# Kernel tuning notes

Hardware: AMD Instinct MI355X
Metric: run time of the kernel (lower is better)

Reference implementation:

```python
import jax, jax.numpy as jnp
import numpy as np

N_NODES = 50000
N_EDGES = 800000
D_FEAT = 128
HIDDEN = 128
BERT_DIM = 768
BATCH = 4096
MAX_ENT = 20
COMB = BERT_DIM + HIDDEN  # 896


def setup_inputs() -> dict:
    key = jax.random.key(0)
    ks = jax.random.split(key, 12)
    article_bert_embeddings = jax.random.normal(ks[0], (BATCH, BERT_DIM), dtype=jnp.float32)
    x = jax.random.normal(ks[1], (N_NODES, D_FEAT), dtype=jnp.float32)
    edge_index = jax.random.randint(ks[2], (2, N_EDGES), 0, N_NODES, dtype=jnp.int64)
    entity_map = jax.random.randint(ks[3], (BATCH, MAX_ENT), 0, N_NODES, dtype=jnp.int64)
    pad = jax.random.uniform(ks[4], (BATCH, MAX_ENT)) < 0.3
    entity_map = jnp.where(pad, jnp.int64(-1), entity_map)
    s = 1.0 / np.sqrt(D_FEAT)
    W1 = jax.random.normal(ks[5], (D_FEAT, HIDDEN), dtype=jnp.float32) * s
    b1 = jnp.zeros((HIDDEN,), dtype=jnp.float32)
    W2 = jax.random.normal(ks[6], (HIDDEN, HIDDEN), dtype=jnp.float32) * (1.0 / np.sqrt(HIDDEN))
    b2 = jnp.zeros((HIDDEN,), dtype=jnp.float32)
    fc1_w = jax.random.normal(ks[7], (COMB, COMB // 2), dtype=jnp.float32) * (1.0 / np.sqrt(COMB))
    fc1_b = jnp.zeros((COMB // 2,), dtype=jnp.float32)
    fc2_w = jax.random.normal(ks[8], (COMB // 2, 1), dtype=jnp.float32) * (1.0 / np.sqrt(COMB // 2))
    fc2_b = jnp.zeros((1,), dtype=jnp.float32)
    return dict(article_bert_embeddings=article_bert_embeddings, x=x,
                edge_index=edge_index, entity_map=entity_map,
                W1=W1, b1=b1, W2=W2, b2=b2,
                fc1_w=fc1_w, fc1_b=fc1_b, fc2_w=fc2_w, fc2_b=fc2_b)


def _gcn_norm(edge_index, n_nodes):
    # add self loops (PyG GCNConv default) and compute symmetric normalization
    loops = jnp.arange(n_nodes, dtype=edge_index.dtype)
    src = jnp.concatenate([edge_index[0], loops])
    dst = jnp.concatenate([edge_index[1], loops])
    deg = jax.ops.segment_sum(jnp.ones_like(dst, dtype=jnp.float32), dst, num_segments=n_nodes)
    dinv = jnp.where(deg > 0, jax.lax.rsqrt(deg), 0.0)
    norm = dinv[src] * dinv[dst]  # [E+N]
    return src, dst, norm


def _gcn_conv(h, W, b, src, dst, norm, n_nodes):
    h = h @ W                                   # [N, H] transform first (cheaper)
    msg = h[src] * norm[:, None]                # [E+N, H] gather
    out = jax.ops.segment_sum(msg, dst, num_segments=n_nodes)
    return out + b


def reference(article_bert_embeddings, x, edge_index, entity_map,
              W1, b1, W2, b2, fc1_w, fc1_b, fc2_w, fc2_b):
    n = x.shape[0]
    src, dst, norm = _gcn_norm(edge_index, n)
    # GNN (dropout in eval mode = identity)
    h = jax.nn.relu(_gcn_conv(x, W1, b1, src, dst, norm, n))
    h = jax.nn.relu(_gcn_conv(h, W2, b2, src, dst, norm, n))
    # ragged mean over entity lists (-1 = padding), fully vectorized
    mask = entity_map >= 0                           # [B, M]
    safe_ids = jnp.where(mask, entity_map, 0)
    gathered = h[safe_ids] * mask[..., None]         # [B, M, H]
    cnt = jnp.maximum(mask.sum(axis=1, keepdims=True).astype(h.dtype), 1.0)
    batch_gnn = gathered.sum(axis=1) / cnt           # [B, H]; rows w/ no entities stay 0
    combined = jnp.concatenate([article_bert_embeddings, batch_gnn], axis=1)
    z = jax.nn.relu(combined @ fc1_w + fc1_b)
    logits = z @ fc2_w + fc2_b
    return jax.nn.sigmoid(logits)
```

## Files before the change

kernel.cpp:

```cpp
#include <hip/hip_runtime.h>
#include <math.h>

typedef __bf16 bf16_t;
typedef __bf16 bfrag8 __attribute__((ext_vector_type(8)));
typedef float  facc4  __attribute__((ext_vector_type(4)));
typedef float  f32x2  __attribute__((ext_vector_type(2)));

#define NBUCK 512
#define BCAP  4096

__device__ inline unsigned short f2b(float x) {
    unsigned int u = __float_as_uint(x);
    unsigned int r = (u + 0x7fffu + ((u >> 16) & 1u)) >> 16;
    return (unsigned short)r;
}
__device__ inline unsigned int pack2(float lo, float hi) {
    return (unsigned int)f2b(lo) | ((unsigned int)f2b(hi) << 16);
}
__device__ inline float blo(unsigned int q) { return __uint_as_float(q << 16); }
__device__ inline float bhi(unsigned int q) { return __uint_as_float(q & 0xffff0000u); }

#if __has_builtin(__builtin_amdgcn_cvt_pk_f32_fp8) && __has_builtin(__builtin_amdgcn_cvt_pk_fp8_f32)
#define HW_FP8 1
#endif

__device__ inline f32x2 fp8pair_dec(unsigned short v) {
#ifdef HW_FP8
    return __builtin_amdgcn_cvt_pk_f32_fp8((int)(unsigned int)v, false);
#else
    f32x2 r;
    unsigned char b0 = (unsigned char)(v & 0xff), b1 = (unsigned char)(v >> 8);
    {
        int e = (b0 >> 3) & 0xf, m = b0 & 7;
        float mag = e ? ldexpf(8.f + m, e - 10) : ldexpf((float)m, -9);
        r.x = (b0 & 0x80) ? -mag : mag;
    }
    {
        int e = (b1 >> 3) & 0xf, m = b1 & 7;
        float mag = e ? ldexpf(8.f + m, e - 10) : ldexpf((float)m, -9);
        r.y = (b1 & 0x80) ? -mag : mag;
    }
    return r;
#endif
}
__device__ inline unsigned char fp8_enc(float x) {
#ifdef HW_FP8
    return (unsigned char)(__builtin_amdgcn_cvt_pk_fp8_f32(x, x, 0, false) & 0xff);
#else
    unsigned char s = (x < 0.f) ? 0x80 : 0;
    float ax = fabsf(x);
    if (!(ax > 0.f)) return s;
    if (ax >= 448.f) return s | 0x7e;
    if (ax < 0.015625f) {
        int q = (int)rintf(ax * 512.f);
        return s | (unsigned char)q;
    }
    int e; float m = frexpf(ax, &e);
    int q = (int)rintf(m * 16.f);
    int E = e - 1;
    if (q == 16) { q = 8; ++E; }
    if (E > 8) return s | 0x7e;
    return s | (unsigned char)(((E + 7) << 3) | (q - 8));
#endif
}

__device__ inline int bucket_of(int d, int N) {
    return (int)(((long long)d * NBUCK) / N);
}

__global__ __launch_bounds__(256) void k_bin2(const int* __restrict__ src,
                                              const int* __restrict__ dst,
                                              int* __restrict__ bcnt,
                                              unsigned int* __restrict__ ebuf,
                                              int E, int N) {
    __shared__ unsigned int sorted[4096];
    __shared__ int hist[NBUCK];
    __shared__ int lstart[NBUCK];
    __shared__ int gbase[NBUCK];
    __shared__ int sm[256];
    int tid = threadIdx.x;
    int base = blockIdx.x * 4096;
    int cnt = min(4096, E - base);
    hist[tid] = 0; hist[tid + 256] = 0;
    __syncthreads();
    unsigned int mye[16]; int myb[16];
#pragma unroll
    for (int i = 0; i < 16; ++i) {
        int idx = i * 256 + tid;
        myb[i] = -1;
        if (idx < cnt) {
            int e = base + idx;
            int s = src[e], d = dst[e];
            mye[i] = ((unsigned int)s << 16) | (unsigned int)d;
            int b = bucket_of(d, N);
            myb[i] = b;
            atomicAdd(&hist[b], 1);
        }
    }
    __syncthreads();
    int p0 = hist[2 * tid], p1 = hist[2 * tid + 1];
    sm[tid] = p0 + p1;
    __syncthreads();
    for (int off = 1; off < 256; off <<= 1) {
        int x = (tid >= off) ? sm[tid - off] : 0;
        __syncthreads();
        sm[tid] += x;
        __syncthreads();
    }
    int excl = sm[tid] - (p0 + p1);
    lstart[2 * tid] = excl;
    lstart[2 * tid + 1] = excl + p0;
    __syncthreads();
    hist[tid] = lstart[tid]; hist[tid + 256] = lstart[tid + 256];
    __syncthreads();
#pragma unroll
    for (int i = 0; i < 16; ++i) {
        if (myb[i] >= 0) {
            int pos = atomicAdd(&hist[myb[i]], 1);
            sorted[pos] = mye[i];
        }
    }
    __syncthreads();
    for (int b = tid; b < NBUCK; b += 256) {
        int c = hist[b] - lstart[b];
        gbase[b] = (c > 0) ? atomicAdd(&bcnt[b], c) : 0;
    }
    __syncthreads();
    for (int idx = tid; idx < cnt; idx += 256) {
        unsigned int v = sorted[idx];
        int b = bucket_of((int)(v & 0xffffu), N);
        ebuf[(size_t)b * BCAP + gbase[b] + (idx - lstart[b])] = v;
    }
}

__global__ __launch_bounds__(256) void k_build2(const unsigned int* __restrict__ ebuf,
                                                const int* __restrict__ bcnt,
                                                int* __restrict__ offs,
                                                float* __restrict__ dinv,
                                                unsigned short* __restrict__ csr,
                                                int N, int E) {
    __shared__ unsigned short seg[BCAP];
    __shared__ int cnt_l[128];
    __shared__ int scan_l[128];
    __shared__ int curs[128];
    __shared__ int smr[256];
    int b = blockIdx.x, tid = threadIdx.x;
    int part = 0;
    for (int j = tid; j < b; j += 256) part += bcnt[j];
    smr[tid] = part;
    __syncthreads();
    for (int off = 128; off > 0; off >>= 1) {
        if (tid < off) smr[tid] += smr[tid + off];
        __syncthreads();
    }
    int base = smr[0];
    int lo = (int)(((long long)b * N + NBUCK - 1) / NBUCK);
    int cnt = bcnt[b];
    int nrange = (int)(((long long)(b + 1) * N + NBUCK - 1) / NBUCK) - lo;
    if (b == 0 && tid == 0) offs[N] = E;
    if (tid < 128) cnt_l[tid] = 0;
    __syncthreads();
    for (int i = tid; i < cnt; i += 256) {
        unsigned int v = ebuf[(size_t)b * BCAP + i];
        atomicAdd(&cnt_l[(int)(v & 0xffffu) - lo], 1);
    }
    __syncthreads();
    if (tid < 128) scan_l[tid] = cnt_l[tid];
    __syncthreads();
    for (int off = 1; off < 128; off <<= 1) {
        int x = 0;
        if (tid < 128 && tid >= off) x = scan_l[tid - off];
        __syncthreads();
        if (tid < 128) scan_l[tid] += x;
        __syncthreads();
    }
    if (tid < 128) {
        int excl = scan_l[tid] - cnt_l[tid];
        curs[tid] = excl;
        if (tid < nrange) {
            offs[lo + tid] = base + excl;
            dinv[lo + tid] = rsqrtf((float)(cnt_l[tid] + 1));
        }
    }
    __syncthreads();
    for (int i = tid; i < cnt; i += 256) {
        unsigned int v = ebuf[(size_t)b * BCAP + i];
        int d = (int)(v & 0xffffu) - lo;
        int p = atomicAdd(&curs[d], 1);
        seg[p] = (unsigned short)(v >> 16);
    }
    __syncthreads();
    for (int i = tid; i < cnt; i += 256) csr[base + i] = seg[i];
}

__global__ __launch_bounds__(256) void k_prep(const float* __restrict__ bert,
                                              unsigned int* __restrict__ bertb, int n8,
                                              const float* __restrict__ W1,
                                              unsigned short* __restrict__ w1t,
                                              const float* __restrict__ W2,
                                              unsigned short* __restrict__ w2t,
                                              const float* __restrict__ Wf,
                                              unsigned short* __restrict__ fwt,
                                              int* __restrict__ bcnt,
                                              float* __restrict__ logacc) {
    __shared__ float tile[64][65];
    int ncvt = (n8 + 255) / 256;
    int bb = blockIdx.x, tid = threadIdx.x;
    if (bb < ncvt) {
        int i = bb * 256 + tid;
        if (i >= n8) return;
        const float4* p = (const float4*)bert + (size_t)i * 2;
        float4 a = p[0], b = p[1];
        uint4 o;
        o.x = pack2(a.x, a.y);
        o.y = pack2(a.z, a.w);
        o.z = pack2(b.x, b.y);
        o.w = pack2(b.z, b.w);
        ((uint4*)bertb)[i] = o;
        return;
    }
    bb -= ncvt;
    if (bb < 128) {
        int i = bb * 256 + tid;
        const float* W = (i < 16384) ? W1 : W2;
        unsigned short* Wt = (i < 16384) ? w1t : w2t;
        int idx = i & 16383;
        int n = idx >> 7, k = idx & 127;
        Wt[idx] = f2b(W[k * 128 + n]);
        return;
    }
    bb -= 128;
    if (bb < 98) {
        int n0 = (bb % 7) * 64, k0 = (bb / 7) * 64;
#pragma unroll
        for (int i = 0; i < 16; ++i) {
            int idx = i * 256 + tid;
            int r = idx >> 6, c = idx & 63;
            tile[r][c] = Wf[(size_t)(k0 + r) * 448 + n0 + c];
        }
        __syncthreads();
#pragma unroll
        for (int i = 0; i < 16; ++i) {
            int idx = i * 256 + tid;
            int c = idx >> 6, r = idx & 63;
            fwt[(size_t)(n0 + c) * 896 + k0 + r] = f2b(tile[r][c]);
        }
        return;
    }
    if (tid < 256) { bcnt[tid] = 0; bcnt[tid + 256] = 0; }
#pragma unroll
    for (int i = 0; i < 16; ++i) logacc[i * 256 + tid] = 0.f;
}

__global__ __launch_bounds__(256) void k_gemm_f32a(const float* __restrict__ A,
                                                   const bf16_t* __restrict__ Bt,
                                                   const float* __restrict__ rs,
                                                   unsigned char* __restrict__ out8, int M) {
    __shared__ bf16_t As[64 * 136];
    __shared__ bf16_t Bs[128 * 136];
    int t = threadIdx.x;
    int wave = t >> 6, lane = t & 63, quad = lane >> 4, l16 = lane & 15;
    int r0 = blockIdx.x * 64;
#pragma unroll
    for (int i = 0; i < 4; ++i) {
        int chunk = t + i * 256;
        int row = chunk >> 4, c8 = (chunk & 15) << 3;
        int gr = r0 + row;
        float4 a0 = make_float4(0.f, 0.f, 0.f, 0.f), a1 = a0;
        if (gr < M) {
            a0 = *(const float4*)&A[(size_t)gr * 128 + c8];
            a1 = *(const float4*)&A[(size_t)gr * 128 + c8 + 4];
        }
        *(uint4*)&As[row * 136 + c8] =
            make_uint4(pack2(a0.x, a0.y), pack2(a0.z, a0.w),
                       pack2(a1.x, a1.y), pack2(a1.z, a1.w));
    }
#pragma unroll
    for (int i = 0; i < 8; ++i) {
        int chunk = t + i * 256;
        int row = chunk >> 4, c8 = (chunk & 15) << 3;
        *(uint4*)&Bs[row * 136 + c8] = *(const uint4*)&Bt[row * 128 + c8];
    }
    __syncthreads();

    facc4 acc[8];
#pragma unroll
    for (int nt = 0; nt < 8; ++nt) acc[nt] = (facc4){0.f, 0.f, 0.f, 0.f};
    int arow = (wave << 4) + l16;
#pragma unroll
    for (int ks = 0; ks < 4; ++ks) {
        int kk = ks * 32 + quad * 8;
        bfrag8 af = *(const bfrag8*)&As[arow * 136 + kk];
#pragma unroll
        for (int nt = 0; nt < 8; ++nt) {
            bfrag8 bf = *(const bfrag8*)&Bs[(nt * 16 + l16) * 136 + kk];
            acc[nt] = __builtin_amdgcn_mfma_f32_16x16x32_bf16(af, bf, acc[nt], 0, 0, 0);
        }
    }
    __syncthreads();
    unsigned char* f8t = (unsigned char*)As;
    int wrow0 = (wave << 4) + quad * 4;
#pragma unroll
    for (int r = 0; r < 4; ++r) {
        int row = wrow0 + r;
        float sc = rs[min(r0 + row, M - 1)];
#pragma unroll
        for (int nt = 0; nt < 8; ++nt)
            f8t[row * 128 + nt * 16 + l16] = fp8_enc(acc[nt][r] * sc);
    }
    __syncthreads();
#pragma unroll
    for (int i = 0; i < 2; ++i) {
        int idx = t + i * 256;
        int row = idx >> 3, cc = (idx & 7) << 4;
        int gr = r0 + row;
        if (gr < M) *(uint4*)&out8[(size_t)gr * 128 + cc] = *(const uint4*)&f8t[row * 128 + cc];
    }
}

__global__ __launch_bounds__(256) void k_gemm_nn128(const bf16_t* __restrict__ A,
                                                    const bf16_t* __restrict__ Bt,
                                                    const float* __restrict__ rs,
                                                    unsigned char* __restrict__ out8, int M) {
    __shared__ bf16_t As[64 * 136];
    __shared__ bf16_t Bs[128 * 136];
    int t = threadIdx.x;
    int wave = t >> 6, lane = t & 63, quad = lane >> 4, l16 = lane & 15;
    int r0 = blockIdx.x * 64;
#pragma unroll
    for (int i = 0; i < 4; ++i) {
        int chunk = t + i * 256;
        int row = chunk >> 4, c8 = (chunk & 15) << 3;
        int gr = r0 + row;
        uint4 v = make_uint4(0u, 0u, 0u, 0u);
        if (gr < M) v = *(const uint4*)&A[(size_t)gr * 128 + c8];
        *(uint4*)&As[row * 136 + c8] = v;
    }
#pragma unroll
    for (int i = 0; i < 8; ++i) {
        int chunk = t + i * 256;
        int row = chunk >> 4, c8 = (chunk & 15) << 3;
        *(uint4*)&Bs[row * 136 + c8] = *(const uint4*)&Bt[row * 128 + c8];
    }
    __syncthreads();

    facc4 acc[8];
#pragma unroll
    for (int nt = 0; nt < 8; ++nt) acc[nt] = (facc4){0.f, 0.f, 0.f, 0.f};
    int arow = (wave << 4) + l16;
#pragma unroll
    for (int ks = 0; ks < 4; ++ks) {
        int kk = ks * 32 + quad * 8;
        bfrag8 af = *(const bfrag8*)&As[arow * 136 + kk];
#pragma unroll
        for (int nt = 0; nt < 8; ++nt) {
            bfrag8 bf = *(const bfrag8*)&Bs[(nt * 16 + l16) * 136 + kk];
            acc[nt] = __builtin_amdgcn_mfma_f32_16x16x32_bf16(af, bf, acc[nt], 0, 0, 0);
        }
    }
    __syncthreads();
    unsigned char* f8t = (unsigned char*)As;
    int wrow0 = (wave << 4) + quad * 4;
#pragma unroll
    for (int r = 0; r < 4; ++r) {
        int row = wrow0 + r;
        float sc = rs[min(r0 + row, M - 1)];
#pragma unroll
        for (int nt = 0; nt < 8; ++nt)
            f8t[row * 128 + nt * 16 + l16] = fp8_enc(acc[nt][r] * sc);
    }
    __syncthreads();
#pragma unroll
    for (int i = 0; i < 2; ++i) {
        int idx = t + i * 256;
        int row = idx >> 3, cc = (idx & 7) << 4;
        int gr = r0 + row;
        if (gr < M) *(uint4*)&out8[(size_t)gr * 128 + cc] = *(const uint4*)&f8t[row * 128 + cc];
    }
}

__global__ __launch_bounds__(256) void k_agg_b(const unsigned short* __restrict__ hx8,
                                               const unsigned short* __restrict__ csr,
                                               const int* __restrict__ offs,
                                               const float* __restrict__ dinv,
                                               const float* __restrict__ bias,
                                               unsigned int* __restrict__ out, int N) {
    int node = blockIdx.x * 4 + (threadIdx.x >> 6);
    int lane = threadIdx.x & 63;
    if (node >= N) return;
    float di = dinv[node];
    f32x2 sf = fp8pair_dec(hx8[(size_t)node * 64 + lane]);
    float acc0 = sf.x, acc1 = sf.y;
    int s0 = offs[node], s1 = offs[node + 1];
    for (int base = s0; base < s1; base += 64) {
        int nloc = min(64, s1 - base);
        int en = 0;
        if (lane < nloc) en = (int)csr[base + lane];
        int j = 0;
        for (; j + 16 <= nloc; j += 16) {
            int sid[16]; unsigned short g[16];
#pragma unroll
            for (int u = 0; u < 16; ++u) sid[u] = __shfl(en, j + u, 64);
#pragma unroll
            for (int u = 0; u < 16; ++u) g[u] = hx8[(size_t)sid[u] * 64 + lane];
#pragma unroll
            for (int u = 0; u < 16; ++u) { f32x2 d = fp8pair_dec(g[u]); acc0 += d.x; acc1 += d.y; }
        }
        for (; j + 4 <= nloc; j += 4) {
            int sid[4]; unsigned short g[4];
#pragma unroll
            for (int u = 0; u < 4; ++u) sid[u] = __shfl(en, j + u, 64);
#pragma unroll
            for (int u = 0; u < 4; ++u) g[u] = hx8[(size_t)sid[u] * 64 + lane];
#pragma unroll
            for (int u = 0; u < 4; ++u) { f32x2 d = fp8pair_dec(g[u]); acc0 += d.x; acc1 += d.y; }
        }
        for (; j < nloc; ++j) {
            int srcn = __shfl(en, j, 64);
            f32x2 d = fp8pair_dec(hx8[(size_t)srcn * 64 + lane]);
            acc0 += d.x; acc1 += d.y;
        }
    }
    float2 bb = *(const float2*)&bias[lane * 2];
    float v0 = fmaxf(acc0 * di + bb.x, 0.f);
    float v1 = fmaxf(acc1 * di + bb.y, 0.f);
    out[(size_t)node * 64 + lane] = pack2(v0, v1);
}

__global__ __launch_bounds__(256) void k_pool_b(const unsigned int* __restrict__ h,
                                                const int* __restrict__ ent,
                                                unsigned int* __restrict__ out) {
    int r = blockIdx.x * 4 + (threadIdx.x >> 6);
    int lane = threadIdx.x & 63;
    float a0 = 0.f, a1 = 0.f;
    int cnt = 0;
#pragma unroll
    for (int m = 0; m < 20; ++m) {
        int id = ent[r * 20 + m];
        if (id >= 0) {
            unsigned int q = h[(size_t)id * 64 + lane];
            a0 += blo(q); a1 += bhi(q); cnt++;
        }
    }
    float inv = 1.f / (float)max(cnt, 1);
    out[(size_t)r * 64 + lane] = pack2(a0 * inv, a1 * inv);
}

__global__ __launch_bounds__(256) void k_mlp1_mfma(const bf16_t* __restrict__ bertb,
                                                   const bf16_t* __restrict__ gnnb,
                                                   const bf16_t* __restrict__ fwt,
                                                   const float* __restrict__ fb,
                                                   const float* __restrict__ w2,
                                                   float* __restrict__ logacc) {
    __shared__ bf16_t As[64 * 136];
    __shared__ bf16_t Bs[64 * 136];
    int t = threadIdx.x;
    int wave = t >> 6, lane = t & 63, quad = lane >> 4, l16 = lane & 15;
    int r0 = blockIdx.x * 64, c0 = blockIdx.y * 64;
    facc4 acc[4];
#pragma unroll
    for (int nt = 0; nt < 4; ++nt) acc[nt] = (facc4){0.f, 0.f, 0.f, 0.f};

    for (int ks = 0; ks < 7; ++ks) {
#pragma unroll
        for (int i = 0; i < 4; ++i) {
            int chunk = t + i * 256;
            int row = chunk >> 4, c8 = (chunk & 15) << 3;
            int gr = r0 + row;
            const bf16_t* srcp = (ks < 6) ? &bertb[(size_t)gr * 768 + ks * 128 + c8]
                                          : &gnnb[(size_t)gr * 128 + c8];
            *(uint4*)&As[row * 136 + c8] = *(const uint4*)srcp;
        }
#pragma unroll
        for (int i = 0; i < 4; ++i) {
            int chunk = t + i * 256;
            int row = chunk >> 4, c8 = (chunk & 15) << 3;
            *(uint4*)&Bs[row * 136 + c8] =
                *(const uint4*)&fwt[(size_t)(c0 + row) * 896 + ks * 128 + c8];
        }
        __syncthreads();
        int arow = (wave << 4) + l16;
#pragma unroll
        for (int sub = 0; sub < 4; ++sub) {
            int kk = sub * 32 + quad * 8;
            bfrag8 af = *(const bfrag8*)&As[arow * 136 + kk];
#pragma unroll
            for (int nt = 0; nt < 4; ++nt) {
                bfrag8 bf = *(const bfrag8*)&Bs[(nt * 16 + l16) * 136 + kk];
                acc[nt] = __builtin_amdgcn_mfma_f32_16x16x32_bf16(af, bf, acc[nt], 0, 0, 0);
            }
        }
        __syncthreads();
    }
    int rbase = r0 + (wave << 4) + quad * 4;
    float part[4] = {0.f, 0.f, 0.f, 0.f};
#pragma unroll
    for (int nt = 0; nt < 4; ++nt) {
        int col = c0 + nt * 16 + l16;
        float bb = fb[col];
        float ww = w2[col];
#pragma unroll
        for (int r = 0; r < 4; ++r)
            part[r] += fmaxf(acc[nt][r] + bb, 0.f) * ww;
    }
#pragma unroll
    for (int m = 8; m >= 1; m >>= 1) {
#pragma unroll
        for (int r = 0; r < 4; ++r) part[r] += __shfl_xor(part[r], m, 64);
    }
    if (l16 == 0) {
#pragma unroll
        for (int r = 0; r < 4; ++r) atomicAdd(&logacc[rbase + r], part[r]);
    }
}

__global__ void k_sig(const float* __restrict__ logacc, const float* __restrict__ b,
                      float* __restrict__ out, int B) {
    int i = blockIdx.x * 256 + threadIdx.x;
    if (i < B) out[i] = 1.f / (1.f + expf(-(logacc[i] + b[0])));
}

extern "C" void kernel_launch(void* const* d_in, const int* in_sizes, int n_in,
                              void* d_out, int out_size, void* d_ws, size_t ws_size,
                              hipStream_t stream) {
    const float* bert = (const float*)d_in[0];
    const float* x    = (const float*)d_in[1];
    const int*   ei   = (const int*)d_in[2];
    const int*   ent  = (const int*)d_in[3];
    const float* W1   = (const float*)d_in[4];
    const float* b1   = (const float*)d_in[5];
    const float* W2   = (const float*)d_in[6];
    const float* b2   = (const float*)d_in[7];
    const float* fc1w = (const float*)d_in[8];
    const float* fc1b = (const float*)d_in[9];
    const float* fc2w = (const float*)d_in[10];
    const float* fc2b = (const float*)d_in[11];
    float* out = (float*)d_out;

    const int N = in_sizes[1] / 128;
    const int E = in_sizes[2] / 2;
    const int B = in_sizes[0] / 768;

    const int* srcv = ei;
    const int* dstv = ei + E;

    char* wsp = (char*)d_ws;
    size_t off = 0;
    auto alloc = [&](size_t bytes) -> void* {
        void* p = wsp + off;
        off += (bytes + 255) & ~(size_t)255;
        return p;
    };
    float* dinv   = (float*)alloc((size_t)N * 4);
    int*   offs   = (int*)alloc((size_t)(N + 1) * 4);
    int*   bcnt   = (int*)alloc(NBUCK * 4);
    float* logacc = (float*)alloc((size_t)B * 4);
    unsigned int*   ebuf  = (unsigned int*)alloc((size_t)NBUCK * BCAP * 4);
    unsigned short* csr16 = (unsigned short*)alloc((size_t)E * 2);
    bf16_t* bertb = (bf16_t*)alloc((size_t)B * 768 * 2);
    bf16_t* w1t   = (bf16_t*)alloc(128 * 128 * 2);
    bf16_t* w2t   = (bf16_t*)alloc(128 * 128 * 2);
    bf16_t* fwt   = (bf16_t*)alloc((size_t)896 * 448 * 2);
    unsigned char* g8buf = (unsigned char*)alloc((size_t)N * 128);
    bf16_t* hbuf  = (bf16_t*)alloc((size_t)N * 128 * 2);
    bf16_t* gnnb  = (bf16_t*)alloc((size_t)B * 128 * 2);
    (void)ws_size; (void)n_in; (void)out_size;

    int nb8 = B * 768 / 8;
    int ncvt = (nb8 + 255) / 256;
    int nprep = ncvt + 128 + 98 + 1;
    k_prep<<<nprep, 256, 0, stream>>>(bert, (unsigned int*)bertb, nb8,
                                      W1, (unsigned short*)w1t, W2, (unsigned short*)w2t,
                                      fc1w, (unsigned short*)fwt, bcnt, logacc);
    k_bin2  <<<(E + 4095) / 4096, 256, 0, stream>>>(srcv, dstv, bcnt, ebuf, E, N);
    k_build2<<<NBUCK, 256, 0, stream>>>(ebuf, bcnt, offs, dinv, csr16, N, E);

    int gb = (N + 63) / 64;
    k_gemm_f32a<<<gb, 256, 0, stream>>>(x, w1t, dinv, g8buf, N);
    k_agg_b<<<(N + 3) / 4, 256, 0, stream>>>((const unsigned short*)g8buf, csr16, offs, dinv, b1,
                                             (unsigned int*)hbuf, N);
    k_gemm_nn128<<<gb, 256, 0, stream>>>(hbuf, w2t, dinv, g8buf, N);
    k_agg_b<<<(N + 3) / 4, 256, 0, stream>>>((const unsigned short*)g8buf, csr16, offs, dinv, b2,
                                             (unsigned int*)hbuf, N);
    k_pool_b<<<B / 4, 256, 0, stream>>>((const unsigned int*)hbuf, ent, (unsigned int*)gnnb);
    k_mlp1_mfma<<<dim3(B / 64, 7), 256, 0, stream>>>(bertb, gnnb, fwt, fc1b, fc2w, logacc);
    k_sig<<<(B + 255) / 256, 256, 0, stream>>>(logacc, fc2b, out, B);
}
```

Measured before the change: 217.2 us.

## Overlap first GEMM with CSR build and fuse layer-1 aggregation into GEMM2

The first feature GEMM no longer depends on dinv. Its output is stored unscaled, and the source-side degree scaling moves into the aggregation as per-edge dinv factors. That lets its tiles be split across the edge-binning and CSR-build kernels as extra blocks, overlapping independent work and removing a launch. The layer-1 aggregation is fused into the layer-2 GEMM: each block aggregates 64 nodes into shared memory and then multiplies by W2, which removes the bf16 hidden buffer round trip and another launch. The costs are an extra dinv gather per edge, larger shared memory for the combined kernels (which can lower occupancy), and a fused aggregation that only runs 4 waves per 64 nodes, so there is less parallelism for latency hiding.

```diff
diff --git a/kernel.cpp b/kernel.cpp
--- a/kernel.cpp
+++ b/kernel.cpp
@@ -68,18 +68,19 @@
     return (int)(((long long)d * NBUCK) / N);
 }
 
-__global__ __launch_bounds__(256) void k_bin2(const int* __restrict__ src,
-                                              const int* __restrict__ dst,
-                                              int* __restrict__ bcnt,
-                                              unsigned int* __restrict__ ebuf,
-                                              int E, int N) {
-    __shared__ unsigned int sorted[4096];
-    __shared__ int hist[NBUCK];
-    __shared__ int lstart[NBUCK];
-    __shared__ int gbase[NBUCK];
-    __shared__ int sm[256];
+
+__device__ inline void bin2_body(char* smem, const int* __restrict__ src,
+                                 const int* __restrict__ dst,
+                                 int* __restrict__ bcnt,
+                                 unsigned int* __restrict__ ebuf,
+                                 int E, int N, int bb) {
+    unsigned int* sorted = (unsigned int*)smem;
+    int* hist   = (int*)(smem + 16384);
+    int* lstart = (int*)(smem + 18432);
+    int* gbase  = (int*)(smem + 20480);
+    int* sm     = (int*)(smem + 22528);
     int tid = threadIdx.x;
-    int base = blockIdx.x * 4096;
+    int base = bb * 4096;
     int cnt = min(4096, E - base);
     hist[tid] = 0; hist[tid + 256] = 0;
     __syncthreads();
@@ -133,18 +134,18 @@
     }
 }
 
-__global__ __launch_bounds__(256) void k_build2(const unsigned int* __restrict__ ebuf,
-                                                const int* __restrict__ bcnt,
-                                                int* __restrict__ offs,
-                                                float* __restrict__ dinv,
-                                                unsigned short* __restrict__ csr,
-                                                int N, int E) {
-    __shared__ unsigned short seg[BCAP];
-    __shared__ int cnt_l[128];
-    __shared__ int scan_l[128];
-    __shared__ int curs[128];
-    __shared__ int smr[256];
-    int b = blockIdx.x, tid = threadIdx.x;
+__device__ inline void build2_body(char* smem, const unsigned int* __restrict__ ebuf,
+                                   const int* __restrict__ bcnt,
+                                   int* __restrict__ offs,
+                                   float* __restrict__ dinv,
+                                   unsigned short* __restrict__ csr,
+                                   int N, int E, int b) {
+    unsigned short* seg = (unsigned short*)smem;
+    int* cnt_l  = (int*)(smem + 8192);
+    int* scan_l = (int*)(smem + 8704);
+    int* curs   = (int*)(smem + 9216);
+    int* smr    = (int*)(smem + 9728);
+    int tid = threadIdx.x;
     int part = 0;
     for (int j = tid; j < b; j += 256) part += bcnt[j];
     smr[tid] = part;
@@ -191,6 +192,103 @@
     }
     __syncthreads();
     for (int i = tid; i < cnt; i += 256) csr[base + i] = seg[i];
+}
+
+__device__ inline void gemm1_body(char* smem, const float* __restrict__ A,
+                                  const bf16_t* __restrict__ Bt,
+                                  unsigned char* __restrict__ out8, int M, int bb) {
+    bf16_t* As = (bf16_t*)smem;
+    bf16_t* Bs = (bf16_t*)(smem + 17408);
+    int t = threadIdx.x;
+    int wave = t >> 6, lane = t & 63, quad = lane >> 4, l16 = lane & 15;
+    int r0 = bb * 64;
+#pragma unroll
+    for (int i = 0; i < 4; ++i) {
+        int chunk = t + i * 256;
+        int row = chunk >> 4, c8 = (chunk & 15) << 3;
+        int gr = r0 + row;
+        float4 a0 = make_float4(0.f, 0.f, 0.f, 0.f), a1 = a0;
+        if (gr < M) {
+            a0 = *(const float4*)&A[(size_t)gr * 128 + c8];
+            a1 = *(const float4*)&A[(size_t)gr * 128 + c8 + 4];
+        }
+        *(uint4*)&As[row * 136 + c8] =
+            make_uint4(pack2(a0.x, a0.y), pack2(a0.z, a0.w),
+                       pack2(a1.x, a1.y), pack2(a1.z, a1.w));
+    }
+#pragma unroll
+    for (int i = 0; i < 8; ++i) {
+        int chunk = t + i * 256;
+        int row = chunk >> 4, c8 = (chunk & 15) << 3;
+        *(uint4*)&Bs[row * 136 + c8] = *(const uint4*)&Bt[row * 128 + c8];
+    }
+    __syncthreads();
+
+    facc4 acc[8];
+#pragma unroll
+    for (int nt = 0; nt < 8; ++nt) acc[nt] = (facc4){0.f, 0.f, 0.f, 0.f};
+    int arow = (wave << 4) + l16;
+#pragma unroll
+    for (int ks = 0; ks < 4; ++ks) {
+        int kk = ks * 32 + quad * 8;
+        bfrag8 af = *(const bfrag8*)&As[arow * 136 + kk];
+#pragma unroll
+        for (int nt = 0; nt < 8; ++nt) {
+            bfrag8 bf = *(const bfrag8*)&Bs[(nt * 16 + l16) * 136 + kk];
+            acc[nt] = __builtin_amdgcn_mfma_f32_16x16x32_bf16(af, bf, acc[nt], 0, 0, 0);
+        }
+    }
+    __syncthreads();
+    unsigned char* f8t = (unsigned char*)As;
+    int wrow0 = (wave << 4) + quad * 4;
+#pragma unroll
+    for (int r = 0; r < 4; ++r) {
+        int row = wrow0 + r;
+#pragma unroll
+        for (int nt = 0; nt < 8; ++nt)
+            f8t[row * 128 + nt * 16 + l16] = fp8_enc(acc[nt][r]);
+    }
+    __syncthreads();
+#pragma unroll
+    for (int i = 0; i < 2; ++i) {
+        int idx = t + i * 256;
+        int row = idx >> 3, cc = (idx & 7) << 4;
+        int gr = r0 + row;
+        if (gr < M) *(uint4*)&out8[(size_t)gr * 128 + cc] = *(const uint4*)&f8t[row * 128 + cc];
+    }
+}
+
+__global__ __launch_bounds__(256) void k_bin_gemm(const int* __restrict__ src,
+                                                  const int* __restrict__ dst,
+                                                  int* __restrict__ bcnt,
+                                                  unsigned int* __restrict__ ebuf,
+                                                  int E, int N,
+                                                  const float* __restrict__ A,
+                                                  const bf16_t* __restrict__ Bt,
+                                                  unsigned char* __restrict__ out8,
+                                                  int nbin) {
+    __shared__ __align__(16) char smem[52224];
+    if ((int)blockIdx.x < nbin)
+        bin2_body(smem, src, dst, bcnt, ebuf, E, N, blockIdx.x);
+    else
+        gemm1_body(smem, A, Bt, out8, N, blockIdx.x - nbin);
+}
+
+__global__ __launch_bounds__(256) void k_build_gemm(const unsigned int* __restrict__ ebuf,
+                                                    const int* __restrict__ bcnt,
+                                                    int* __restrict__ offs,
+                                                    float* __restrict__ dinv,
+                                                    unsigned short* __restrict__ csr,
+                                                    int N, int E,
+                                                    const float* __restrict__ A,
+                                                    const bf16_t* __restrict__ Bt,
+                                                    unsigned char* __restrict__ out8,
+                                                    int tile0) {
+    __shared__ __align__(16) char smem[52224];
+    if ((int)blockIdx.x < NBUCK)
+        build2_body(smem, ebuf, bcnt, offs, dinv, csr, N, E, blockIdx.x);
+    else
+        gemm1_body(smem, A, Bt, out8, N, blockIdx.x - NBUCK + tile0);
 }
 
 __global__ __launch_bounds__(256) void k_prep(const float* __restrict__ bert,
@@ -252,37 +350,82 @@
     for (int i = 0; i < 16; ++i) logacc[i * 256 + tid] = 0.f;
 }
 
-__global__ __launch_bounds__(256) void k_gemm_f32a(const float* __restrict__ A,
-                                                   const bf16_t* __restrict__ Bt,
-                                                   const float* __restrict__ rs,
-                                                   unsigned char* __restrict__ out8, int M) {
+__global__ __launch_bounds__(256) void k_aggmm(const unsigned short* __restrict__ hx8,
+                                               const unsigned short* __restrict__ csr,
+                                               const int* __restrict__ offs,
+                                               const float* __restrict__ dinv,
+                                               const float* __restrict__ bias1,
+                                               const bf16_t* __restrict__ W2t,
+                                               unsigned char* __restrict__ out8, int N) {
     __shared__ bf16_t As[64 * 136];
     __shared__ bf16_t Bs[128 * 136];
     int t = threadIdx.x;
     int wave = t >> 6, lane = t & 63, quad = lane >> 4, l16 = lane & 15;
     int r0 = blockIdx.x * 64;
 #pragma unroll
-    for (int i = 0; i < 4; ++i) {
-        int chunk = t + i * 256;
-        int row = chunk >> 4, c8 = (chunk & 15) << 3;
-        int gr = r0 + row;
-        float4 a0 = make_float4(0.f, 0.f, 0.f, 0.f), a1 = a0;
-        if (gr < M) {
-            a0 = *(const float4*)&A[(size_t)gr * 128 + c8];
-            a1 = *(const float4*)&A[(size_t)gr * 128 + c8 + 4];
-        }
-        *(uint4*)&As[row * 136 + c8] =
-            make_uint4(pack2(a0.x, a0.y), pack2(a0.z, a0.w),
-                       pack2(a1.x, a1.y), pack2(a1.z, a1.w));
-    }
-#pragma unroll
     for (int i = 0; i < 8; ++i) {
         int chunk = t + i * 256;
         int row = chunk >> 4, c8 = (chunk & 15) << 3;
-        *(uint4*)&Bs[row * 136 + c8] = *(const uint4*)&Bt[row * 128 + c8];
-    }
-    __syncthreads();
-
+        *(uint4*)&Bs[row * 136 + c8] = *(const uint4*)&W2t[row * 128 + c8];
+    }
+    float2 b2v = *(const float2*)&bias1[lane * 2];
+    for (int i = 0; i < 16; ++i) {
+        int row = (wave << 4) + i;
+        int node = r0 + row;
+        float v0 = 0.f, v1 = 0.f;
+        if (node < N) {
+            float di = dinv[node];
+            f32x2 sf = fp8pair_dec(hx8[(size_t)node * 64 + lane]);
+            float acc0 = sf.x * di, acc1 = sf.y * di;
+            int s0 = offs[node], s1 = offs[node + 1];
+            for (int eb = s0; eb < s1; eb += 64) {
+                int nloc = min(64, s1 - eb);
+                int en = 0; float dvl = 0.f;
+                if (lane < nloc) { en = (int)csr[eb + lane]; dvl = dinv[en]; }
+                int j = 0;
+                for (; j + 16 <= nloc; j += 16) {
+                    int sid[16]; float dv[16]; unsigned short g[16];
+#pragma unroll
+                    for (int u = 0; u < 16; ++u) {
+                        sid[u] = __shfl(en, j + u, 64);
+                        dv[u]  = __shfl(dvl, j + u, 64);
+                    }
+#pragma unroll
+                    for (int u = 0; u < 16; ++u) g[u] = hx8[(size_t)sid[u] * 64 + lane];
+#pragma unroll
+                    for (int u = 0; u < 16; ++u) {
+                        f32x2 d = fp8pair_dec(g[u]);
+                        acc0 += d.x * dv[u]; acc1 += d.y * dv[u];
+                    }
+                }
+                for (; j + 4 <= nloc; j += 4) {
+                    int sid[4]; float dv[4]; unsigned short g[4];
+#pragma unroll
+                    for (int u = 0; u < 4; ++u) {
+                        sid[u] = __shfl(en, j + u, 64);
+                        dv[u]  = __shfl(dvl, j + u, 64);
+                    }
+#pragma unroll
+                    for (int u = 0; u < 4; ++u) g[u] = hx8[(size_t)sid[u] * 64 + lane];
+#pragma unroll
+                    for (int u = 0; u < 4; ++u) {
+                        f32x2 d = fp8pair_dec(g[u]);
+                        acc0 += d.x * dv[u]; acc1 += d.y * dv[u];
+                    }
+                }
+                for (; j < nloc; ++j) {
+                    int sn = __shfl(en, j, 64);
+                    float dv = __shfl(dvl, j, 64);
+                    f32x2 d = fp8pair_dec(hx8[(size_t)sn * 64 + lane]);
+                    acc0 += d.x * dv; acc1 += d.y * dv;
+                }
+            }
+            v0 = fmaxf(acc0 * di + b2v.x, 0.f);
+            v1 = fmaxf(acc1 * di + b2v.y, 0.f);
+        }
+        *(unsigned int*)&As[row * 136 + lane * 2] = pack2(v0, v1);
+    }
+    __syncthreads();
     facc4 acc[8];
 #pragma unroll
     for (int nt = 0; nt < 8; ++nt) acc[nt] = (facc4){0.f, 0.f, 0.f, 0.f};
@@ -303,7 +446,7 @@
 #pragma unroll
     for (int r = 0; r < 4; ++r) {
         int row = wrow0 + r;
-        float sc = rs[min(r0 + row, M - 1)];
+        float sc = dinv[min(r0 + row, N - 1)];
 #pragma unroll
         for (int nt = 0; nt < 8; ++nt)
             f8t[row * 128 + nt * 16 + l16] = fp8_enc(acc[nt][r] * sc);
@@ -314,68 +457,7 @@
         int idx = t + i * 256;
         int row = idx >> 3, cc = (idx & 7) << 4;
         int gr = r0 + row;
-        if (gr < M) *(uint4*)&out8[(size_t)gr * 128 + cc] = *(const uint4*)&f8t[row * 128 + cc];
-    }
-}
-
-__global__ __launch_bounds__(256) void k_gemm_nn128(const bf16_t* __restrict__ A,
-                                                    const bf16_t* __restrict__ Bt,
-                                                    const float* __restrict__ rs,
-                                                    unsigned char* __restrict__ out8, int M) {
-    __shared__ bf16_t As[64 * 136];
-    __shared__ bf16_t Bs[128 * 136];
-    int t = threadIdx.x;
-    int wave = t >> 6, lane = t & 63, quad = lane >> 4, l16 = lane & 15;
-    int r0 = blockIdx.x * 64;
-#pragma unroll
-    for (int i = 0; i < 4; ++i) {
-        int chunk = t + i * 256;
-        int row = chunk >> 4, c8 = (chunk & 15) << 3;
-        int gr = r0 + row;
-        uint4 v = make_uint4(0u, 0u, 0u, 0u);
-        if (gr < M) v = *(const uint4*)&A[(size_t)gr * 128 + c8];
-        *(uint4*)&As[row * 136 + c8] = v;
-    }
-#pragma unroll
-    for (int i = 0; i < 8; ++i) {
-        int chunk = t + i * 256;
-        int row = chunk >> 4, c8 = (chunk & 15) << 3;
-        *(uint4*)&Bs[row * 136 + c8] = *(const uint4*)&Bt[row * 128 + c8];
-    }
-    __syncthreads();
-
-    facc4 acc[8];
-#pragma unroll
-    for (int nt = 0; nt < 8; ++nt) acc[nt] = (facc4){0.f, 0.f, 0.f, 0.f};
-    int arow = (wave << 4) + l16;
-#pragma unroll
-    for (int ks = 0; ks < 4; ++ks) {
-        int kk = ks * 32 + quad * 8;
-        bfrag8 af = *(const bfrag8*)&As[arow * 136 + kk];
-#pragma unroll
-        for (int nt = 0; nt < 8; ++nt) {
-            bfrag8 bf = *(const bfrag8*)&Bs[(nt * 16 + l16) * 136 + kk];
-            acc[nt] = __builtin_amdgcn_mfma_f32_16x16x32_bf16(af, bf, acc[nt], 0, 0, 0);
-        }
-    }
-    __syncthreads();
-    unsigned char* f8t = (unsigned char*)As;
-    int wrow0 = (wave << 4) + quad * 4;
-#pragma unroll
-    for (int r = 0; r < 4; ++r) {
-        int row = wrow0 + r;
-        float sc = rs[min(r0 + row, M - 1)];
-#pragma unroll
-        for (int nt = 0; nt < 8; ++nt)
-            f8t[row * 128 + nt * 16 + l16] = fp8_enc(acc[nt][r] * sc);
-    }
-    __syncthreads();
-#pragma unroll
-    for (int i = 0; i < 2; ++i) {
-        int idx = t + i * 256;
-        int row = idx >> 3, cc = (idx & 7) << 4;
-        int gr = r0 + row;
-        if (gr < M) *(uint4*)&out8[(size_t)gr * 128 + cc] = *(const uint4*)&f8t[row * 128 + cc];
+        if (gr < N) *(uint4*)&out8[(size_t)gr * 128 + cc] = *(const uint4*)&f8t[row * 128 + cc];
     }
 }
 
@@ -561,7 +643,8 @@
     bf16_t* w1t   = (bf16_t*)alloc(128 * 128 * 2);
     bf16_t* w2t   = (bf16_t*)alloc(128 * 128 * 2);
     bf16_t* fwt   = (bf16_t*)alloc((size_t)896 * 448 * 2);
-    unsigned char* g8buf = (unsigned char*)alloc((size_t)N * 128);
+    unsigned char* g8a = (unsigned char*)alloc((size_t)N * 128);
+    unsigned char* g8b = (unsigned char*)alloc((size_t)N * 128);
     bf16_t* hbuf  = (bf16_t*)alloc((size_t)N * 128 * 2);
     bf16_t* gnnb  = (bf16_t*)alloc((size_t)B * 128 * 2);
     (void)ws_size; (void)n_in; (void)out_size;
@@ -569,18 +652,20 @@
     int nb8 = B * 768 / 8;
     int ncvt = (nb8 + 255) / 256;
     int nprep = ncvt + 128 + 98 + 1;
+    int nbin = (E + 4095) / 4096;
+    int gb = (N + 63) / 64;
+    int g1a = gb / 2, g1b = gb - g1a;
+
     k_prep<<<nprep, 256, 0, stream>>>(bert, (unsigned int*)bertb, nb8,
                                       W1, (unsigned short*)w1t, W2, (unsigned short*)w2t,
                                       fc1w, (unsigned short*)fwt, bcnt, logacc);
-    k_bin2  <<<(E + 4095) / 4096, 256, 0, stream>>>(srcv, dstv, bcnt, ebuf, E, N);
-    k_build2<<<NBUCK, 256, 0, stream>>>(ebuf, bcnt, offs, dinv, csr16, N, E);
-
-    int gb = (N + 63) / 64;
-    k_gemm_f32a<<<gb, 256, 0, stream>>>(x, w1t, dinv, g8buf, N);
-    k_agg_b<<<(N + 3) / 4, 256, 0, stream>>>((const unsigned short*)g8buf, csr16, offs, dinv, b1,
-                                             (unsigned int*)hbuf, N);
-    k_gemm_nn128<<<gb, 256, 0, stream>>>(hbuf, w2t, dinv, g8buf, N);
-    k_agg_b<<<(N + 3) / 4, 256, 0, stream>>>((const unsigned short*)g8buf, csr16, offs, dinv, b2,
+    k_bin_gemm<<<nbin + g1a, 256, 0, stream>>>(srcv, dstv, bcnt, ebuf, E, N,
+                                               x, w1t, g8a, nbin);
+    k_build_gemm<<<NBUCK + g1b, 256, 0, stream>>>(ebuf, bcnt, offs, dinv, csr16, N, E,
+                                                  x, w1t, g8a, g1a);
+    k_aggmm<<<gb, 256, 0, stream>>>((const unsigned short*)g8a, csr16, offs, dinv, b1,
+                                    w2t, g8b, N);
+    k_agg_b<<<(N + 3) / 4, 256, 0, stream>>>((const unsigned short*)g8b, csr16, offs, dinv, b2,
                                              (unsigned int*)hbuf, N);
     k_pool_b<<<B / 4, 256, 0, stream>>>((const unsigned int*)hbuf, ent, (unsigned int*)gnnb);
     k_mlp1_mfma<<<dim3(B / 64, 7), 256, 0, stream>>>(bertb, gnnb, fwt, fc1b, fc2w, logacc);
```

After: 242.4 us. 1.12x slower.
